# Kernel optimization log

Measured on AMD Instinct MI355X. Metric: run time of the kernel, lower is better.

## Reference

```python
import jax, jax.numpy as jnp
import numpy as np

N = 100000   # num_nodes
E = 1600000  # num_edges
DIN = 128
H1 = 256
H2 = 128
SLOPE = 0.01  # torch leaky_relu default negative slope


def _gcn_conv(h, W, b, src, dst):
    # GCNConv: add self-loops, symmetric deg^-1/2 normalization, linear transform, scatter-add, bias
    hw = h @ W  # [N, out]
    loops = jnp.arange(N)
    s = jnp.concatenate([src, loops])
    d = jnp.concatenate([dst, loops])
    deg = jax.ops.segment_sum(jnp.ones(s.shape[0], dtype=hw.dtype), d, num_segments=N)
    dis = jnp.where(deg > 0, jax.lax.rsqrt(deg), 0.0)
    msg = hw[s] * (dis[s] * dis[d])[:, None]
    return jax.ops.segment_sum(msg, d, num_segments=N) + b


def _gru_cell(x, h, Wih, Whh, bih, bhh):
    # torch.nn.GRUCell semantics; weight layout [3H, in], gate order r, z, n
    gi = x @ Wih.T + bih
    gh = h @ Whh.T + bhh
    ir, iz, inn = jnp.split(gi, 3, axis=-1)
    hr, hz, hn = jnp.split(gh, 3, axis=-1)
    r = jax.nn.sigmoid(ir + hr)
    z = jax.nn.sigmoid(iz + hz)
    n = jnp.tanh(inn + r * hn)
    return (1.0 - z) * n + z * h


def setup_inputs() -> dict:
    key = jax.random.key(0)
    ks = jax.random.split(key, 24)
    rn = lambda k, shape, s=0.05: (jax.random.normal(k, shape) * s).astype(jnp.float32)
    return {
        "x": rn(ks[0], (N, DIN), 1.0),
        "edge_index": jax.random.randint(ks[1], (2, E), 0, N, dtype=jnp.int32),
        "prev0": rn(ks[2], (N, H1), 1.0),
        "prev1": rn(ks[3], (N, H2), 1.0),
        "Wp1": rn(ks[4], (DIN, 256)), "bp1": jnp.zeros((256,), jnp.float32),
        "Wp2": rn(ks[5], (256, 128)), "bp2": jnp.zeros((128,), jnp.float32),
        "Wc1": rn(ks[6], (128, H1)), "bc1": jnp.zeros((H1,), jnp.float32),
        "Wc2": rn(ks[7], (H1, H2)), "bc2": jnp.zeros((H2,), jnp.float32),
        "Wih1": rn(ks[8], (3 * H1, H1)), "Whh1": rn(ks[9], (3 * H1, H1)),
        "bih1": jnp.zeros((3 * H1,), jnp.float32), "bhh1": jnp.zeros((3 * H1,), jnp.float32),
        "Wih2": rn(ks[10], (3 * H2, H2)), "Whh2": rn(ks[11], (3 * H2, H2)),
        "bih2": jnp.zeros((3 * H2,), jnp.float32), "bhh2": jnp.zeros((3 * H2,), jnp.float32),
        "Wpost": rn(ks[12], (H2, 2)), "bpost": jnp.zeros((2,), jnp.float32),
    }


def reference(x, edge_index, prev0, prev1, Wp1, bp1, Wp2, bp2, Wc1, bc1, Wc2, bc2,
              Wih1, Whh1, bih1, bhh1, Wih2, Whh2, bih2, bhh2, Wpost, bpost):
    src, dst = edge_index[0], edge_index[1]
    # preprocess MLP (dropout p=0 => identity)
    h = jax.nn.leaky_relu(x @ Wp1 + bp1, SLOPE)
    h = jax.nn.leaky_relu(h @ Wp2 + bp2, SLOPE)
    # GCN layer 1 + GRU temporal update
    h = jax.nn.leaky_relu(_gcn_conv(h, Wc1, bc1, src, dst), SLOPE)
    h = _gru_cell(h, prev0, Wih1, Whh1, bih1, bhh1)
    emb0 = h
    # GCN layer 2 + GRU temporal update
    h = jax.nn.leaky_relu(_gcn_conv(h, Wc2, bc2, src, dst), SLOPE)
    h = _gru_cell(h, prev1, Wih2, Whh2, bih2, bhh2)
    emb1 = h
    # postprocess and reduce
    out = jnp.sum(h @ Wpost + bpost, axis=-1)  # [N]
    return out, emb0, emb1
```

## Files before the change

### kernel.cpp

```cpp
#include <hip/hip_runtime.h>
#include <cstdint>
#include <cstddef>

typedef __bf16 bf16x8 __attribute__((ext_vector_type(8)));
typedef float f32x4 __attribute__((ext_vector_type(4)));
typedef unsigned short us16;

__device__ __forceinline__ float lrelu(float v) { return v >= 0.0f ? v : 0.01f * v; }
__device__ __forceinline__ float fsigmoid(float x) {
  x = fminf(fmaxf(x, -30.0f), 30.0f);
  return 1.0f / (1.0f + __expf(-x));
}
__device__ __forceinline__ float ftanh(float x) {
  x = fminf(fmaxf(x, -15.0f), 15.0f);
  float e = __expf(2.0f * x);
  return (e - 1.0f) / (e + 1.0f);
}
__device__ __forceinline__ us16 f2b(float f) {
  unsigned int u = __builtin_bit_cast(unsigned int, f);
  u = (u + 0x7fffu + ((u >> 16) & 1u)) >> 16;
  return (us16)u;
}
__device__ __forceinline__ float b2f(us16 h) {
  unsigned int u = ((unsigned int)h) << 16;
  return __builtin_bit_cast(float, u);
}
__device__ __forceinline__ unsigned pk2(float a, float b) {
  return (unsigned)f2b(a) | ((unsigned)f2b(b) << 16);
}
__device__ __forceinline__ void unp8(int4 v, float* t) {
  unsigned a = (unsigned)v.x, b = (unsigned)v.y, c = (unsigned)v.z, d = (unsigned)v.w;
  t[0] = b2f((us16)(a & 0xffff)); t[1] = b2f((us16)(a >> 16));
  t[2] = b2f((us16)(b & 0xffff)); t[3] = b2f((us16)(b >> 16));
  t[4] = b2f((us16)(c & 0xffff)); t[5] = b2f((us16)(c >> 16));
  t[6] = b2f((us16)(d & 0xffff)); t[7] = b2f((us16)(d >> 16));
}

__device__ __forceinline__ void stage16(const us16* gsrc, us16* ldst) {
  __builtin_amdgcn_global_load_lds(
      (const __attribute__((address_space(1))) unsigned int*)(const void*)gsrc,
      (__attribute__((address_space(3))) unsigned int*)(void*)ldst, 16, 0, 0);
}
__device__ __forceinline__ bf16x8 frag_rd(const us16* base, int row, int byte_in_row) {
  int byte = row * 128 + (byte_in_row ^ ((row & 7) << 4));
  return *(const bf16x8*)((const char*)base + byte);
}
__device__ __forceinline__ bf16x8 frd32(const us16* tilebase, int row, int ck16) {
  int slot = ck16 ^ ((row >> 1) & 3);
  return *(const bf16x8*)(tilebase + row * 32 + slot * 8);
}

__global__ void k_deg(const int* __restrict__ dst, int* __restrict__ indeg, int E) {
  int e = blockIdx.x * 256 + threadIdx.x;
  if (e < E) atomicAdd(&indeg[dst[e]], 1);
}

__global__ __launch_bounds__(1024) void k_scan1(const int* __restrict__ v, int* __restrict__ rp,
                                                int* __restrict__ part, float* __restrict__ dis, int n) {
  __shared__ int wsum[16];
  int base = blockIdx.x << 10;
  int t = threadIdx.x, lane = t & 63, wv = t >> 6;
  int val = (base + t < n) ? v[base + t] : 0;
  if (base + t < n) dis[base + t] = rsqrtf((float)(val + 1));
  int s = val;
  #pragma unroll
  for (int off = 1; off < 64; off <<= 1) {
    int u = __shfl_up(s, off);
    if (lane >= off) s += u;
  }
  if (lane == 63) wsum[wv] = s;
  __syncthreads();
  int wadd = 0;
  #pragma unroll
  for (int w = 0; w < 16; ++w) wadd += (w < wv) ? wsum[w] : 0;
  if (base + t < n) rp[base + t] = wadd + s - val;
  if (t == 0) {
    int tot = 0;
    #pragma unroll
    for (int w = 0; w < 16; ++w) tot += wsum[w];
    part[blockIdx.x] = tot;
  }
}

__global__ __launch_bounds__(1024) void k_scan2(int* __restrict__ p, int nc) {
  __shared__ int wsum[16];
  int t = threadIdx.x, lane = t & 63, wv = t >> 6;
  int val = (t < nc) ? p[t] : 0;
  int s = val;
  #pragma unroll
  for (int off = 1; off < 64; off <<= 1) {
    int u = __shfl_up(s, off);
    if (lane >= off) s += u;
  }
  if (lane == 63) wsum[wv] = s;
  __syncthreads();
  int wadd = 0;
  #pragma unroll
  for (int w = 0; w < 16; ++w) wadd += (w < wv) ? wsum[w] : 0;
  if (t < nc) p[t] = wadd + s - val;
}

__global__ void k_scan3(int* __restrict__ rp, const int* __restrict__ part,
                        int* __restrict__ cursor, int n, int total) {
  int i = blockIdx.x * 256 + threadIdx.x;
  if (i < n) {
    int v = rp[i] + part[i >> 10];
    rp[i] = v;
    cursor[i] = v;
  } else if (i == n) {
    rp[n] = total;
  }
}

__global__ void k_fill(const int* __restrict__ src, const int* __restrict__ dst,
                       const float* __restrict__ dis, int* __restrict__ cursor,
                       int* __restrict__ csrc, float* __restrict__ cw, int E) {
  int e = blockIdx.x * 256 + threadIdx.x;
  if (e >= E) return;
  int s = src[e], d = dst[e];
  int pos = atomicAdd(&cursor[d], 1);
  csrc[pos] = s;
  cw[pos] = dis[s] * dis[d];
}

__global__ void k_cast(const float* __restrict__ in, us16* __restrict__ out, int n) {
  int i = (blockIdx.x * 256 + threadIdx.x) * 4;
  if (i >= n) return;
  float4 v = *(const float4*)(in + i);
  *(ushort4*)(out + i) = make_ushort4(f2b(v.x), f2b(v.y), f2b(v.z), f2b(v.w));
}

__global__ void k_prepw(const float* __restrict__ Wih1, const float* __restrict__ Whh1,
                        const float* __restrict__ Wih2, const float* __restrict__ Whh2,
                        const float* __restrict__ Wp1, const float* __restrict__ Wp2,
                        const float* __restrict__ Wc1, const float* __restrict__ Wc2,
                        us16* __restrict__ Wih1b, us16* __restrict__ Whh1b,
                        us16* __restrict__ Wih2b, us16* __restrict__ Whh2b,
                        us16* __restrict__ WtP1, us16* __restrict__ WtP2,
                        us16* __restrict__ WtC1, us16* __restrict__ WtC2) {
  int e = blockIdx.x * 256 + threadIdx.x;
  if (e < 196608) { Wih1b[e] = f2b(Wih1[e]); return; }
  e -= 196608;
  if (e < 196608) { Whh1b[e] = f2b(Whh1[e]); return; }
  e -= 196608;
  if (e < 49152) { Wih2b[e] = f2b(Wih2[e]); return; }
  e -= 49152;
  if (e < 49152) { Whh2b[e] = f2b(Whh2[e]); return; }
  e -= 49152;
  if (e < 32768) { int r = e & 127, c = e >> 7; WtP1[e] = f2b(Wp1[(size_t)r * 256 + c]); return; }
  e -= 32768;
  if (e < 32768) { int r = e & 255, c = e >> 8; WtP2[e] = f2b(Wp2[(size_t)r * 128 + c]); return; }
  e -= 32768;
  if (e < 32768) { int r = e & 127, c = e >> 7; WtC1[e] = f2b(Wc1[(size_t)r * 256 + c]); return; }
  e -= 32768;
  if (e < 32768) { int r = e & 255, c = e >> 8; WtC2[e] = f2b(Wc2[(size_t)r * 128 + c]); }
}

template<int ACT, int BIAS>
__global__ __launch_bounds__(256) void k_mm(const us16* __restrict__ A,
                                            const us16* __restrict__ Bt,
                                            const float* __restrict__ bias,
                                            us16* __restrict__ Cb,
                                            int M, int K, int Nc, int ny) {
  __shared__ __align__(16) us16 lds[2][2 * 8192];
  const int bm = (blockIdx.x / ny) * 128;
  const int bn = (blockIdx.x % ny) * 128;
  const int tid = threadIdx.x;
  const int lane = tid & 63;
  const int wave = tid >> 6;
  const int wm = (wave >> 1) * 64;
  const int wn = (wave & 1) * 64;
  const int lr = lane & 15;
  const int lk = lane >> 4;
  const int srow = lane >> 3;
  const int schk = (lane & 7) ^ srow;
  f32x4 acc[4][4] = {};

  auto stage = [&](int k0, us16* buf) {
    #pragma unroll
    for (int it = 0; it < 4; ++it) {
      int r8 = (wave * 4 + it) * 8;
      int ar = bm + r8 + srow; if (ar >= M) ar = M - 1;
      stage16(A + (size_t)ar * K + k0 + schk * 8, buf + r8 * 64);
      stage16(Bt + (size_t)(bn + r8 + srow) * K + k0 + schk * 8, buf + 8192 + r8 * 64);
    }
  };

  const int nk = K >> 6;
  stage(0, lds[0]);
  for (int t = 0; t < nk; ++t) {
    us16* cur = lds[t & 1];
    __syncthreads();
    if (t + 1 < nk) stage((t + 1) << 6, lds[(t + 1) & 1]);
    #pragma unroll
    for (int kk = 0; kk < 2; ++kk) {
      bf16x8 af[4], bq[4];
      #pragma unroll
      for (int i = 0; i < 4; ++i) af[i] = frag_rd(cur, wm + i * 16 + lr, kk * 64 + lk * 16);
      #pragma unroll
      for (int j = 0; j < 4; ++j) bq[j] = frag_rd(cur + 8192, wn + j * 16 + lr, kk * 64 + lk * 16);
      #pragma unroll
      for (int i = 0; i < 4; ++i)
        #pragma unroll
        for (int j = 0; j < 4; ++j)
          acc[i][j] = __builtin_amdgcn_mfma_f32_16x16x32_bf16(af[i], bq[j], acc[i][j], 0, 0, 0);
    }
  }
  float bb[4];
  #pragma unroll
  for (int j = 0; j < 4; ++j) bb[j] = BIAS ? bias[bn + wn + j * 16 + lr] : 0.0f;
  #pragma unroll
  for (int i = 0; i < 4; ++i) {
    #pragma unroll
    for (int q = 0; q < 4; ++q) {
      int row = bm + wm + i * 16 + lk * 4 + q;
      if (row < M) {
        #pragma unroll
        for (int j = 0; j < 4; ++j) {
          int col = bn + wn + j * 16 + lr;
          float v = acc[i][j][q] + bb[j];
          if (ACT) v = lrelu(v);
          Cb[(size_t)row * Nc + col] = f2b(v);
        }
      }
    }
  }
}

template<int ACT>
__global__ __launch_bounds__(256) void k_agg128(const us16* __restrict__ hw, const int* __restrict__ rp,
                                                const int* __restrict__ csrc, const float* __restrict__ cw,
                                                const float* __restrict__ dis, const float* __restrict__ bias,
                                                us16* __restrict__ outp, int M) {
  int node = blockIdx.x * 16 + (threadIdx.x >> 4);
  int l = threadIdx.x & 15;
  if (node >= M) return;
  const us16* base = hw + l * 8;
  float acc[8], t0[8], t1[8], t2[8], t3[8];
  float dn = dis[node];
  float sw = dn * dn;
  {
    int4 v = *(const int4*)(base + (size_t)node * 128);
    unp8(v, t0);
    #pragma unroll
    for (int j = 0; j < 8; ++j) acc[j] = t0[j] * sw;
  }
  int e = rp[node], e1 = rp[node + 1];
  for (; e + 4 <= e1; e += 4) {
    int s0 = csrc[e], s1 = csrc[e + 1], s2 = csrc[e + 2], s3 = csrc[e + 3];
    float w0 = cw[e], w1 = cw[e + 1], w2 = cw[e + 2], w3 = cw[e + 3];
    int4 v0 = *(const int4*)(base + (size_t)s0 * 128);
    int4 v1 = *(const int4*)(base + (size_t)s1 * 128);
    int4 v2 = *(const int4*)(base + (size_t)s2 * 128);
    int4 v3 = *(const int4*)(base + (size_t)s3 * 128);
    unp8(v0, t0); unp8(v1, t1); unp8(v2, t2); unp8(v3, t3);
    #pragma unroll
    for (int j = 0; j < 8; ++j) acc[j] = fmaf(w0, t0[j], acc[j]);
    #pragma unroll
    for (int j = 0; j < 8; ++j) acc[j] = fmaf(w1, t1[j], acc[j]);
    #pragma unroll
    for (int j = 0; j < 8; ++j) acc[j] = fmaf(w2, t2[j], acc[j]);
    #pragma unroll
    for (int j = 0; j < 8; ++j) acc[j] = fmaf(w3, t3[j], acc[j]);
  }
  for (; e < e1; ++e) {
    int s0 = csrc[e];
    float w0 = cw[e];
    int4 v0 = *(const int4*)(base + (size_t)s0 * 128);
    unp8(v0, t0);
    #pragma unroll
    for (int j = 0; j < 8; ++j) acc[j] = fmaf(w0, t0[j], acc[j]);
  }
  if (ACT) {
    float4 b0 = *(const float4*)(bias + l * 8);
    float4 b1 = *(const float4*)(bias + l * 8 + 4);
    float bb[8] = {b0.x, b0.y, b0.z, b0.w, b1.x, b1.y, b1.z, b1.w};
    #pragma unroll
    for (int j = 0; j < 8; ++j) acc[j] = lrelu(acc[j] + bb[j]);
  }
  int4 o;
  o.x = (int)pk2(acc[0], acc[1]);
  o.y = (int)pk2(acc[2], acc[3]);
  o.z = (int)pk2(acc[4], acc[5]);
  o.w = (int)pk2(acc[6], acc[7]);
  *(int4*)(outp + (size_t)node * 128 + l * 8) = o;
}

template<int H, int WB, int PH>
__global__ __launch_bounds__(512) void k_fgru(const us16* __restrict__ xb, const us16* __restrict__ hb,
                                              const us16* __restrict__ Wih, const us16* __restrict__ Whh,
                                              const float* __restrict__ bih, const float* __restrict__ bhh,
                                              float* __restrict__ emb, us16* __restrict__ embb,
                                              const float* __restrict__ Wpost, const float* __restrict__ bpost,
                                              float* __restrict__ outv, int M, int ny) {
  __shared__ __align__(16) us16 lds[2][14336];
  const int nwg = gridDim.x;
  int bid = blockIdx.x;
  {
    int q8 = nwg >> 3, r8 = nwg & 7;
    int xc = bid & 7, ix = bid >> 3;
    bid = (xc < r8 ? xc * (q8 + 1) : r8 * (q8 + 1) + (xc - r8) * q8) + ix;
  }
  const int bn = (bid % ny) * 32;
  const int bm = (bid / ny) * 128;
  const int tid = threadIdx.x;
  const int lane = tid & 63, wave = tid >> 6;
  const int pair = wave >> 1;
  const int role = wave & 1;
  const int wm = pair * 32;
  const int lr = lane & 15, lk = lane >> 4;
  const int sl_row = lane >> 2;
  const int sl_chk = (lane & 3) ^ ((lane >> 3) & 3);

  f32x4 acc[3][2][2] = {};

  auto stage_step = [&](int k0, us16* buf) {
    #pragma unroll
    for (int it = 0; it < 4; ++it) {
      int m = wave * 4 + it;
      if (m >= 28) break;
      const us16* src;
      us16* dst;
      if (m < 16) {
        int r0 = (m & 7) * 16;
        int ar = bm + r0 + sl_row; if (ar >= M) ar = M - 1;
        src = (m < 8 ? xb : hb) + (size_t)ar * H + k0 + sl_chk * 8;
        dst = buf + (m < 8 ? 0 : 4096) + r0 * 32;
      } else {
        int wi = m - 16;
        int g6 = wi >> 1;
        int r0 = (wi & 1) * 16;
        const us16* W = (g6 < 3) ? Wih : Whh;
        int gg = (g6 < 3) ? g6 : g6 - 3;
        src = W + (size_t)(gg * H + bn + r0 + sl_row) * H + k0 + sl_chk * 8;
        dst = buf + 8192 + g6 * 1024 + r0 * 32;
      }
      stage16(src, dst);
    }
  };

  const int nk = H >> 5;
  stage_step(0, lds[0]);
  for (int t = 0; t < nk; ++t) {
    us16* cur = lds[t & 1];
    __syncthreads();
    if (t + 1 < nk) stage_step((t + 1) << 5, lds[(t + 1) & 1]);
    const us16* at = cur + (role ? 4096 : 0);
    bf16x8 a0 = frd32(at, wm + lr, lk);
    bf16x8 a1 = frd32(at, wm + 16 + lr, lk);
    #pragma unroll
    for (int g = 0; g < 3; ++g) {
      const us16* wt = cur + 8192 + (role * 3 + g) * 1024;
      bf16x8 b0 = frd32(wt, lr, lk);
      bf16x8 b1 = frd32(wt, 16 + lr, lk);
      acc[g][0][0] = __builtin_amdgcn_mfma_f32_16x16x32_bf16(a0, b0, acc[g][0][0], 0, 0, 0);
      acc[g][0][1] = __builtin_amdgcn_mfma_f32_16x16x32_bf16(a0, b1, acc[g][0][1], 0, 0, 0);
      acc[g][1][0] = __builtin_amdgcn_mfma_f32_16x16x32_bf16(a1, b0, acc[g][1][0], 0, 0, 0);
      acc[g][1][1] = __builtin_amdgcn_mfma_f32_16x16x32_bf16(a1, b1, acc[g][1][1], 0, 0, 0);
    }
  }
  __syncthreads();
  float* xch = (float*)&lds[0][0];
  if (role) {
    #pragma unroll
    for (int g = 0; g < 3; ++g)
      #pragma unroll
      for (int i = 0; i < 2; ++i)
        #pragma unroll
        for (int j = 0; j < 2; ++j)
          *(f32x4*)&xch[((((pair * 3 + g) * 2 + i) * 2 + j) * 64 + lane) * 4] = acc[g][i][j];
  }
  __syncthreads();
  if (!role) {
    float part[2][4] = {};
    #pragma unroll
    for (int j = 0; j < 2; ++j) {
      int col = bn + j * 16 + lr;
      float bir = bih[col], biz = bih[H + col], bin = bih[2 * H + col];
      float bhr = bhh[col], bhz = bhh[H + col], bhn = bhh[2 * H + col];
      float wps = 0.0f;
      if (PH) wps = Wpost[2 * col] + Wpost[2 * col + 1];
      #pragma unroll
      for (int i = 0; i < 2; ++i) {
        f32x4 gr_ = *(const f32x4*)&xch[((((pair * 3 + 0) * 2 + i) * 2 + j) * 64 + lane) * 4];
        f32x4 gz_ = *(const f32x4*)&xch[((((pair * 3 + 1) * 2 + i) * 2 + j) * 64 + lane) * 4];
        f32x4 gn_ = *(const f32x4*)&xch[((((pair * 3 + 2) * 2 + i) * 2 + j) * 64 + lane) * 4];
        #pragma unroll
        for (int q = 0; q < 4; ++q) {
          int row = bm + wm + i * 16 + lk * 4 + q;
          if (row < M) {
            float r = fsigmoid(acc[0][i][j][q] + bir + gr_[q] + bhr);
            float z = fsigmoid(acc[1][i][j][q] + biz + gz_[q] + bhz);
            float n = ftanh(acc[2][i][j][q] + bin + r * (gn_[q] + bhn));
            float hv = b2f(hb[(size_t)row * H + col]);
            float o = (1.0f - z) * n + z * hv;
            emb[(size_t)row * H + col] = o;
            if (WB) embb[(size_t)row * H + col] = f2b(o);
            if (PH) part[i][q] += o * wps;
          }
        }
      }
    }
    if (PH) {
      float bsum = bpost[0] + bpost[1];
      #pragma unroll
      for (int i = 0; i < 2; ++i)
        #pragma unroll
        for (int q = 0; q < 4; ++q) {
          float v = part[i][q];
          v += __shfl_xor(v, 1); v += __shfl_xor(v, 2);
          v += __shfl_xor(v, 4); v += __shfl_xor(v, 8);
          int row = bm + wm + i * 16 + lk * 4 + q;
          if (lr == 0 && row < M)
            atomicAdd(&outv[row], v + (bn == 0 ? bsum : 0.0f));
        }
    }
  }
}

extern "C" void kernel_launch(void* const* d_in, const int* in_sizes, int n_in,
                              void* d_out, int out_size, void* d_ws, size_t ws_size,
                              hipStream_t stream) {
  const float* x     = (const float*)d_in[0];
  const int*   ei    = (const int*)d_in[1];
  const float* prev0 = (const float*)d_in[2];
  const float* prev1 = (const float*)d_in[3];
  const float* Wp1   = (const float*)d_in[4];
  const float* bp1   = (const float*)d_in[5];
  const float* Wp2   = (const float*)d_in[6];
  const float* bp2   = (const float*)d_in[7];
  const float* Wc1   = (const float*)d_in[8];
  const float* bc1   = (const float*)d_in[9];
  const float* Wc2   = (const float*)d_in[10];
  const float* bc2   = (const float*)d_in[11];
  const float* Wih1  = (const float*)d_in[12];
  const float* Whh1  = (const float*)d_in[13];
  const float* bih1  = (const float*)d_in[14];
  const float* bhh1  = (const float*)d_in[15];
  const float* Wih2  = (const float*)d_in[16];
  const float* Whh2  = (const float*)d_in[17];
  const float* bih2  = (const float*)d_in[18];
  const float* bhh2  = (const float*)d_in[19];
  const float* Wpost = (const float*)d_in[20];
  const float* bpost = (const float*)d_in[21];

  const int N = in_sizes[0] / 128;
  const int E = in_sizes[1] / 2;
  const int* srcp = ei;
  const int* dstp = ei + E;

  char* wsb = (char*)d_ws;
  size_t off = 0;
  auto alloc = [&](size_t bytes) -> void* {
    void* p = wsb + off;
    off = (off + bytes + 255) & ~(size_t)255;
    return p;
  };
  float* dis    = (float*)alloc((size_t)N * 4);
  int*   indeg  = (int*)alloc((size_t)N * 4);
  int*   rp     = (int*)alloc((size_t)(N + 1) * 4);
  int*   part   = (int*)alloc((size_t)1024 * 4);
  int*   cursor = (int*)alloc((size_t)N * 4);
  int*   csrc   = (int*)alloc((size_t)E * 4);
  float* cw     = (float*)alloc((size_t)E * 4);
  us16* xb    = (us16*)alloc((size_t)N * 128 * 2);
  us16* p0b   = (us16*)alloc((size_t)N * 256 * 2);
  us16* p1b   = (us16*)alloc((size_t)N * 128 * 2);
  us16* WtP1  = (us16*)alloc((size_t)256 * 128 * 2);
  us16* WtP2  = (us16*)alloc((size_t)128 * 256 * 2);
  us16* WtC1  = (us16*)alloc((size_t)256 * 128 * 2);
  us16* WtC2  = (us16*)alloc((size_t)128 * 256 * 2);
  us16* Wih1b = (us16*)alloc((size_t)768 * 256 * 2);
  us16* Whh1b = (us16*)alloc((size_t)768 * 256 * 2);
  us16* Wih2b = (us16*)alloc((size_t)384 * 128 * 2);
  us16* Whh2b = (us16*)alloc((size_t)384 * 128 * 2);
  us16* bufA  = (us16*)alloc((size_t)N * 256 * 2);
  us16* bufB  = (us16*)alloc((size_t)N * 128 * 2);
  us16* bufD  = (us16*)alloc((size_t)N * 128 * 2);
  us16* emb0b = (us16*)alloc((size_t)N * 256 * 2);
  (void)ws_size; (void)n_in; (void)out_size;

  float* outv = (float*)d_out;
  float* emb0 = outv + N;
  float* emb1 = emb0 + (size_t)N * 256;

  auto cg = [](long n) { return (unsigned)((n / 4 + 255) / 256); };

  hipMemsetAsync(outv, 0, (size_t)N * 4, stream);

  k_cast<<<cg((long)N * 128), 256, 0, stream>>>(x, xb, N * 128);
  k_cast<<<cg((long)N * 256), 256, 0, stream>>>(prev0, p0b, N * 256);
  k_cast<<<cg((long)N * 128), 256, 0, stream>>>(prev1, p1b, N * 128);
  k_prepw<<<2432, 256, 0, stream>>>(Wih1, Whh1, Wih2, Whh2, Wp1, Wp2, Wc1, Wc2,
                                    Wih1b, Whh1b, Wih2b, Whh2b, WtP1, WtP2, WtC1, WtC2);

  hipMemsetAsync(indeg, 0, (size_t)N * 4, stream);
  k_deg<<<(E + 255) / 256, 256, 0, stream>>>(dstp, indeg, E);
  const int NC = (N + 1023) / 1024;
  k_scan1<<<NC, 1024, 0, stream>>>(indeg, rp, part, dis, N);
  k_scan2<<<1, 1024, 0, stream>>>(part, NC);
  k_scan3<<<(N + 256) / 256, 256, 0, stream>>>(rp, part, cursor, N, E);
  k_fill<<<(E + 255) / 256, 256, 0, stream>>>(srcp, dstp, dis, cursor, csrc, cw, E);

  const int MB = (N + 127) / 128;
  const int AB = (N + 15) / 16;

  k_mm<1, 1><<<MB * 2, 256, 0, stream>>>(xb, WtP1, bp1, bufA, N, 128, 256, 2);
  k_mm<1, 1><<<MB, 256, 0, stream>>>(bufA, WtP2, bp2, bufB, N, 256, 128, 1);
  k_agg128<0><<<AB, 256, 0, stream>>>(bufB, rp, csrc, cw, dis, nullptr, bufD, N);
  k_mm<1, 1><<<MB * 2, 256, 0, stream>>>(bufD, WtC1, bc1, bufA, N, 128, 256, 2);
  k_fgru<256, 1, 0><<<MB * 8, 512, 0, stream>>>(bufA, p0b, Wih1b, Whh1b, bih1, bhh1,
                                                emb0, emb0b, nullptr, nullptr, nullptr, N, 8);
  k_mm<0, 0><<<MB, 256, 0, stream>>>(emb0b, WtC2, nullptr, bufB, N, 256, 128, 1);
  k_agg128<1><<<AB, 256, 0, stream>>>(bufB, rp, csrc, cw, dis, bc2, bufD, N);
  k_fgru<128, 0, 1><<<MB * 4, 512, 0, stream>>>(bufD, p1b, Wih2b, Whh2b, bih2, bhh2,
                                                emb1, nullptr, Wpost, bpost, outv, N, 4);
}
```

Before: 803.1 us.

## Preload full weight tiles into LDS and stream activations directly from global

Both the dense GEMM kernel and the fused GRU kernel stop double-buffering A and B tiles through LDS with async global-to-LDS loads per K step. Instead, each block loads its entire weight slice into swizzled LDS once, then reads activation fragments straight from global memory into registers across a fully unrolled K loop. This removes the per-step barriers and the LDS round trip for activations. In exchange, LDS use per block grows (up to 96 KB for H=256 GRU), which may cut occupancy, and uncoalesced direct A loads may add global-memory latency with no overlap.

```diff
diff --git a/kernel.cpp b/kernel.cpp
--- a/kernel.cpp
+++ b/kernel.cpp
@@ -34,20 +34,6 @@
   t[2] = b2f((us16)(b & 0xffff)); t[3] = b2f((us16)(b >> 16));
   t[4] = b2f((us16)(c & 0xffff)); t[5] = b2f((us16)(c >> 16));
   t[6] = b2f((us16)(d & 0xffff)); t[7] = b2f((us16)(d >> 16));
-}
-
-__device__ __forceinline__ void stage16(const us16* gsrc, us16* ldst) {
-  __builtin_amdgcn_global_load_lds(
-      (const __attribute__((address_space(1))) unsigned int*)(const void*)gsrc,
-      (__attribute__((address_space(3))) unsigned int*)(void*)ldst, 16, 0, 0);
-}
-__device__ __forceinline__ bf16x8 frag_rd(const us16* base, int row, int byte_in_row) {
-  int byte = row * 128 + (byte_in_row ^ ((row & 7) << 4));
-  return *(const bf16x8*)((const char*)base + byte);
-}
-__device__ __forceinline__ bf16x8 frd32(const us16* tilebase, int row, int ck16) {
-  int slot = ck16 ^ ((row >> 1) & 3);
-  return *(const bf16x8*)(tilebase + row * 32 + slot * 8);
 }
 
 __global__ void k_deg(const int* __restrict__ dst, int* __restrict__ indeg, int E) {
@@ -156,13 +142,13 @@
   if (e < 32768) { int r = e & 255, c = e >> 8; WtC2[e] = f2b(Wc2[(size_t)r * 128 + c]); }
 }
 
-template<int ACT, int BIAS>
+template<int ACT, int BIAS, int K>
 __global__ __launch_bounds__(256) void k_mm(const us16* __restrict__ A,
                                             const us16* __restrict__ Bt,
                                             const float* __restrict__ bias,
                                             us16* __restrict__ Cb,
-                                            int M, int K, int Nc, int ny) {
-  __shared__ __align__(16) us16 lds[2][2 * 8192];
+                                            int M, int Nc, int ny) {
+  __shared__ __align__(16) us16 wl[128 * K];
   const int bm = (blockIdx.x / ny) * 128;
   const int bn = (blockIdx.x % ny) * 128;
   const int tid = threadIdx.x;
@@ -172,39 +158,42 @@
   const int wn = (wave & 1) * 64;
   const int lr = lane & 15;
   const int lk = lane >> 4;
-  const int srow = lane >> 3;
-  const int schk = (lane & 7) ^ srow;
+
+  constexpr int CHB = K / 8;
+  #pragma unroll
+  for (int it = 0; it < (128 * CHB) / 256; ++it) {
+    int idx = it * 256 + tid;
+    int cir = idx & (CHB - 1);
+    int col = idx / CHB;
+    int4 v = *(const int4*)(Bt + (size_t)(bn + col) * K + cir * 8);
+    size_t db = (((size_t)col * K + cir * 8) * 2) ^ (size_t)((col & 7) << 4);
+    *(int4*)((char*)wl + db) = v;
+  }
+  __syncthreads();
+
+  const us16* ap[4];
+  #pragma unroll
+  for (int i = 0; i < 4; ++i) {
+    int r = bm + wm + i * 16 + lr; if (r >= M) r = M - 1;
+    ap[i] = A + (size_t)r * K + lk * 8;
+  }
   f32x4 acc[4][4] = {};
-
-  auto stage = [&](int k0, us16* buf) {
-    #pragma unroll
-    for (int it = 0; it < 4; ++it) {
-      int r8 = (wave * 4 + it) * 8;
-      int ar = bm + r8 + srow; if (ar >= M) ar = M - 1;
-      stage16(A + (size_t)ar * K + k0 + schk * 8, buf + r8 * 64);
-      stage16(Bt + (size_t)(bn + r8 + srow) * K + k0 + schk * 8, buf + 8192 + r8 * 64);
+  #pragma unroll
+  for (int kk = 0; kk < K / 32; ++kk) {
+    bf16x8 af[4], bq[4];
+    #pragma unroll
+    for (int i = 0; i < 4; ++i) af[i] = *(const bf16x8*)(ap[i] + kk * 32);
+    #pragma unroll
+    for (int j = 0; j < 4; ++j) {
+      int col = wn + j * 16 + lr;
+      size_t db = (((size_t)col * K + kk * 32 + lk * 8) * 2) ^ (size_t)((col & 7) << 4);
+      bq[j] = *(const bf16x8*)((const char*)wl + db);
     }
-  };
-
-  const int nk = K >> 6;
-  stage(0, lds[0]);
-  for (int t = 0; t < nk; ++t) {
-    us16* cur = lds[t & 1];
-    __syncthreads();
-    if (t + 1 < nk) stage((t + 1) << 6, lds[(t + 1) & 1]);
-    #pragma unroll
-    for (int kk = 0; kk < 2; ++kk) {
-      bf16x8 af[4], bq[4];
+    #pragma unroll
+    for (int i = 0; i < 4; ++i)
       #pragma unroll
-      for (int i = 0; i < 4; ++i) af[i] = frag_rd(cur, wm + i * 16 + lr, kk * 64 + lk * 16);
-      #pragma unroll
-      for (int j = 0; j < 4; ++j) bq[j] = frag_rd(cur + 8192, wn + j * 16 + lr, kk * 64 + lk * 16);
-      #pragma unroll
-      for (int i = 0; i < 4; ++i)
-        #pragma unroll
-        for (int j = 0; j < 4; ++j)
-          acc[i][j] = __builtin_amdgcn_mfma_f32_16x16x32_bf16(af[i], bq[j], acc[i][j], 0, 0, 0);
-    }
+      for (int j = 0; j < 4; ++j)
+        acc[i][j] = __builtin_amdgcn_mfma_f32_16x16x32_bf16(af[i], bq[j], acc[i][j], 0, 0, 0);
   }
   float bb[4];
   #pragma unroll
@@ -293,7 +282,7 @@
                                               float* __restrict__ emb, us16* __restrict__ embb,
                                               const float* __restrict__ Wpost, const float* __restrict__ bpost,
                                               float* __restrict__ outv, int M, int ny) {
-  __shared__ __align__(16) us16 lds[2][14336];
+  __shared__ __align__(16) us16 wl[192 * H];
   const int nwg = gridDim.x;
   int bid = blockIdx.x;
   {
@@ -307,60 +296,51 @@
   const int lane = tid & 63, wave = tid >> 6;
   const int pair = wave >> 1;
   const int role = wave & 1;
-  const int wm = pair * 32;
   const int lr = lane & 15, lk = lane >> 4;
-  const int sl_row = lane >> 2;
-  const int sl_chk = (lane & 3) ^ ((lane >> 3) & 3);
+
+  constexpr int CHR = H / 8;
+  #pragma unroll
+  for (int it = 0; it < (192 * CHR) / 512; ++it) {
+    int idx = it * 512 + tid;
+    int cir = idx & (CHR - 1);
+    int row = idx / CHR;
+    int g6 = row >> 5, c = row & 31;
+    const us16* W = (g6 < 3) ? Wih : Whh;
+    int gg = (g6 < 3) ? g6 : g6 - 3;
+    int4 v = *(const int4*)(W + (size_t)(gg * H + bn + c) * H + cir * 8);
+    size_t db = (((size_t)row * H + cir * 8) * 2) ^ (size_t)((c & 7) << 4);
+    *(int4*)((char*)wl + db) = v;
+  }
+  __syncthreads();
+
+  const us16* abase = role ? hb : xb;
+  int ra0 = bm + pair * 32 + lr;      if (ra0 >= M) ra0 = M - 1;
+  int ra1 = bm + pair * 32 + 16 + lr; if (ra1 >= M) ra1 = M - 1;
+  const us16* ap0 = abase + (size_t)ra0 * H + lk * 8;
+  const us16* ap1 = abase + (size_t)ra1 * H + lk * 8;
 
   f32x4 acc[3][2][2] = {};
-
-  auto stage_step = [&](int k0, us16* buf) {
-    #pragma unroll
-    for (int it = 0; it < 4; ++it) {
-      int m = wave * 4 + it;
-      if (m >= 28) break;
-      const us16* src;
-      us16* dst;
-      if (m < 16) {
-        int r0 = (m & 7) * 16;
-        int ar = bm + r0 + sl_row; if (ar >= M) ar = M - 1;
-        src = (m < 8 ? xb : hb) + (size_t)ar * H + k0 + sl_chk * 8;
-        dst = buf + (m < 8 ? 0 : 4096) + r0 * 32;
-      } else {
-        int wi = m - 16;
-        int g6 = wi >> 1;
-        int r0 = (wi & 1) * 16;
-        const us16* W = (g6 < 3) ? Wih : Whh;
-        int gg = (g6 < 3) ? g6 : g6 - 3;
-        src = W + (size_t)(gg * H + bn + r0 + sl_row) * H + k0 + sl_chk * 8;
-        dst = buf + 8192 + g6 * 1024 + r0 * 32;
-      }
-      stage16(src, dst);
-    }
-  };
-
-  const int nk = H >> 5;
-  stage_step(0, lds[0]);
-  for (int t = 0; t < nk; ++t) {
-    us16* cur = lds[t & 1];
-    __syncthreads();
-    if (t + 1 < nk) stage_step((t + 1) << 5, lds[(t + 1) & 1]);
-    const us16* at = cur + (role ? 4096 : 0);
-    bf16x8 a0 = frd32(at, wm + lr, lk);
-    bf16x8 a1 = frd32(at, wm + 16 + lr, lk);
+  #pragma unroll
+  for (int t = 0; t < H / 32; ++t) {
+    bf16x8 a0 = *(const bf16x8*)(ap0 + t * 32);
+    bf16x8 a1 = *(const bf16x8*)(ap1 + t * 32);
     #pragma unroll
     for (int g = 0; g < 3; ++g) {
-      const us16* wt = cur + 8192 + (role * 3 + g) * 1024;
-      bf16x8 b0 = frd32(wt, lr, lk);
-      bf16x8 b1 = frd32(wt, 16 + lr, lk);
+      int g6 = role * 3 + g;
+      int c0 = lr, c1 = 16 + lr;
+      size_t db0 = (((size_t)(g6 * 32 + c0) * H + t * 32 + lk * 8) * 2) ^ (size_t)((c0 & 7) << 4);
+      size_t db1 = (((size_t)(g6 * 32 + c1) * H + t * 32 + lk * 8) * 2) ^ (size_t)((c1 & 7) << 4);
+      bf16x8 b0 = *(const bf16x8*)((const char*)wl + db0);
+      bf16x8 b1 = *(const bf16x8*)((const char*)wl + db1);
       acc[g][0][0] = __builtin_amdgcn_mfma_f32_16x16x32_bf16(a0, b0, acc[g][0][0], 0, 0, 0);
       acc[g][0][1] = __builtin_amdgcn_mfma_f32_16x16x32_bf16(a0, b1, acc[g][0][1], 0, 0, 0);
       acc[g][1][0] = __builtin_amdgcn_mfma_f32_16x16x32_bf16(a1, b0, acc[g][1][0], 0, 0, 0);
       acc[g][1][1] = __builtin_amdgcn_mfma_f32_16x16x32_bf16(a1, b1, acc[g][1][1], 0, 0, 0);
     }
   }
-  __syncthreads();
-  float* xch = (float*)&lds[0][0];
+
+  __syncthreads();
+  float* xch = (float*)&wl[0];
   if (role) {
     #pragma unroll
     for (int g = 0; g < 3; ++g)
@@ -387,7 +367,7 @@
         f32x4 gn_ = *(const f32x4*)&xch[((((pair * 3 + 2) * 2 + i) * 2 + j) * 64 + lane) * 4];
         #pragma unroll
         for (int q = 0; q < 4; ++q) {
-          int row = bm + wm + i * 16 + lk * 4 + q;
+          int row = bm + pair * 32 + i * 16 + lk * 4 + q;
           if (row < M) {
             float r = fsigmoid(acc[0][i][j][q] + bir + gr_[q] + bhr);
             float z = fsigmoid(acc[1][i][j][q] + biz + gz_[q] + bhz);
@@ -410,7 +390,7 @@
           float v = part[i][q];
           v += __shfl_xor(v, 1); v += __shfl_xor(v, 2);
           v += __shfl_xor(v, 4); v += __shfl_xor(v, 8);
-          int row = bm + wm + i * 16 + lk * 4 + q;
+          int row = bm + pair * 32 + i * 16 + lk * 4 + q;
           if (lr == 0 && row < M)
             atomicAdd(&outv[row], v + (bn == 0 ? bsum : 0.0f));
         }
@@ -505,13 +485,13 @@
   const int MB = (N + 127) / 128;
   const int AB = (N + 15) / 16;
 
-  k_mm<1, 1><<<MB * 2, 256, 0, stream>>>(xb, WtP1, bp1, bufA, N, 128, 256, 2);
-  k_mm<1, 1><<<MB, 256, 0, stream>>>(bufA, WtP2, bp2, bufB, N, 256, 128, 1);
+  k_mm<1, 1, 128><<<MB * 2, 256, 0, stream>>>(xb, WtP1, bp1, bufA, N, 256, 2);
+  k_mm<1, 1, 256><<<MB, 256, 0, stream>>>(bufA, WtP2, bp2, bufB, N, 128, 1);
   k_agg128<0><<<AB, 256, 0, stream>>>(bufB, rp, csrc, cw, dis, nullptr, bufD, N);
-  k_mm<1, 1><<<MB * 2, 256, 0, stream>>>(bufD, WtC1, bc1, bufA, N, 128, 256, 2);
+  k_mm<1, 1, 128><<<MB * 2, 256, 0, stream>>>(bufD, WtC1, bc1, bufA, N, 256, 2);
   k_fgru<256, 1, 0><<<MB * 8, 512, 0, stream>>>(bufA, p0b, Wih1b, Whh1b, bih1, bhh1,
                                                 emb0, emb0b, nullptr, nullptr, nullptr, N, 8);
-  k_mm<0, 0><<<MB, 256, 0, stream>>>(emb0b, WtC2, nullptr, bufB, N, 256, 128, 1);
+  k_mm<0, 0, 256><<<MB, 256, 0, stream>>>(emb0b, WtC2, nullptr, bufB, N, 128, 1);
   k_agg128<1><<<AB, 256, 0, stream>>>(bufB, rp, csrc, cw, dis, bc2, bufD, N);
   k_fgru<128, 0, 1><<<MB * 4, 512, 0, stream>>>(bufD, p1b, Wih2b, Whh2b, bih2, bhh2,
                                                 emb1, nullptr, Wpost, bpost, outv, N, 4);
```

Measured after the change: 839.4 us. 1.05x slower.

## Load GRU MFMA operands directly from global memory instead of LDS staging

Applied to the files above, without the earlier changes.

The fused GRU kernel drops its double-buffered LDS staging (global_load_lds plus __syncthreads each k-step) and instead has each wave read its A rows and weight rows straight from global memory into MFMA fragments, with a fully unrolled k loop. LDS is now used only for the gate exchange between wave pairs. This removes per-step barriers and LDS traffic, but weight tiles are no longer shared across waves through LDS. Each wave reads them independently, and the reads are 16-byte strided row loads that depend on L1/L2 hits rather than coalesced staging.

```diff
diff --git a/kernel.cpp b/kernel.cpp
--- a/kernel.cpp
+++ b/kernel.cpp
@@ -44,10 +44,6 @@
 __device__ __forceinline__ bf16x8 frag_rd(const us16* base, int row, int byte_in_row) {
   int byte = row * 128 + (byte_in_row ^ ((row & 7) << 4));
   return *(const bf16x8*)((const char*)base + byte);
-}
-__device__ __forceinline__ bf16x8 frd32(const us16* tilebase, int row, int ck16) {
-  int slot = ck16 ^ ((row >> 1) & 3);
-  return *(const bf16x8*)(tilebase + row * 32 + slot * 8);
 }
 
 __global__ void k_deg(const int* __restrict__ dst, int* __restrict__ indeg, int E) {
@@ -293,7 +289,7 @@
                                               float* __restrict__ emb, us16* __restrict__ embb,
                                               const float* __restrict__ Wpost, const float* __restrict__ bpost,
                                               float* __restrict__ outv, int M, int ny) {
-  __shared__ __align__(16) us16 lds[2][14336];
+  __shared__ __align__(16) float xch[12288];
   const int nwg = gridDim.x;
   int bid = blockIdx.x;
   {
@@ -307,60 +303,39 @@
   const int lane = tid & 63, wave = tid >> 6;
   const int pair = wave >> 1;
   const int role = wave & 1;
-  const int wm = pair * 32;
   const int lr = lane & 15, lk = lane >> 4;
-  const int sl_row = lane >> 2;
-  const int sl_chk = (lane & 3) ^ ((lane >> 3) & 3);
+
+  const us16* abase = role ? hb : xb;
+  int ra0 = bm + pair * 32 + lr;      if (ra0 >= M) ra0 = M - 1;
+  int ra1 = bm + pair * 32 + 16 + lr; if (ra1 >= M) ra1 = M - 1;
+  const us16* ap0 = abase + (size_t)ra0 * H + lk * 8;
+  const us16* ap1 = abase + (size_t)ra1 * H + lk * 8;
+  const us16* wbase = role ? Whh : Wih;
+  const us16* bp0[3];
+  const us16* bp1[3];
+  #pragma unroll
+  for (int g = 0; g < 3; ++g) {
+    bp0[g] = wbase + (size_t)(g * H + bn + lr) * H + lk * 8;
+    bp1[g] = wbase + (size_t)(g * H + bn + 16 + lr) * H + lk * 8;
+  }
 
   f32x4 acc[3][2][2] = {};
-
-  auto stage_step = [&](int k0, us16* buf) {
-    #pragma unroll
-    for (int it = 0; it < 4; ++it) {
-      int m = wave * 4 + it;
-      if (m >= 28) break;
-      const us16* src;
-      us16* dst;
-      if (m < 16) {
-        int r0 = (m & 7) * 16;
-        int ar = bm + r0 + sl_row; if (ar >= M) ar = M - 1;
-        src = (m < 8 ? xb : hb) + (size_t)ar * H + k0 + sl_chk * 8;
-        dst = buf + (m < 8 ? 0 : 4096) + r0 * 32;
-      } else {
-        int wi = m - 16;
-        int g6 = wi >> 1;
-        int r0 = (wi & 1) * 16;
-        const us16* W = (g6 < 3) ? Wih : Whh;
-        int gg = (g6 < 3) ? g6 : g6 - 3;
-        src = W + (size_t)(gg * H + bn + r0 + sl_row) * H + k0 + sl_chk * 8;
-        dst = buf + 8192 + g6 * 1024 + r0 * 32;
-      }
-      stage16(src, dst);
-    }
-  };
-
-  const int nk = H >> 5;
-  stage_step(0, lds[0]);
-  for (int t = 0; t < nk; ++t) {
-    us16* cur = lds[t & 1];
-    __syncthreads();
-    if (t + 1 < nk) stage_step((t + 1) << 5, lds[(t + 1) & 1]);
-    const us16* at = cur + (role ? 4096 : 0);
-    bf16x8 a0 = frd32(at, wm + lr, lk);
-    bf16x8 a1 = frd32(at, wm + 16 + lr, lk);
+  #pragma unroll
+  for (int t = 0; t < H / 32; ++t) {
+    bf16x8 a0 = *(const bf16x8*)(ap0 + t * 32);
+    bf16x8 a1 = *(const bf16x8*)(ap1 + t * 32);
     #pragma unroll
     for (int g = 0; g < 3; ++g) {
-      const us16* wt = cur + 8192 + (role * 3 + g) * 1024;
-      bf16x8 b0 = frd32(wt, lr, lk);
-      bf16x8 b1 = frd32(wt, 16 + lr, lk);
+      bf16x8 b0 = *(const bf16x8*)(bp0[g] + t * 32);
+      bf16x8 b1 = *(const bf16x8*)(bp1[g] + t * 32);
       acc[g][0][0] = __builtin_amdgcn_mfma_f32_16x16x32_bf16(a0, b0, acc[g][0][0], 0, 0, 0);
       acc[g][0][1] = __builtin_amdgcn_mfma_f32_16x16x32_bf16(a0, b1, acc[g][0][1], 0, 0, 0);
       acc[g][1][0] = __builtin_amdgcn_mfma_f32_16x16x32_bf16(a1, b0, acc[g][1][0], 0, 0, 0);
       acc[g][1][1] = __builtin_amdgcn_mfma_f32_16x16x32_bf16(a1, b1, acc[g][1][1], 0, 0, 0);
     }
   }
+
   __syncthreads();
-  float* xch = (float*)&lds[0][0];
   if (role) {
     #pragma unroll
     for (int g = 0; g < 3; ++g)
@@ -387,7 +362,7 @@
         f32x4 gn_ = *(const f32x4*)&xch[((((pair * 3 + 2) * 2 + i) * 2 + j) * 64 + lane) * 4];
         #pragma unroll
         for (int q = 0; q < 4; ++q) {
-          int row = bm + wm + i * 16 + lk * 4 + q;
+          int row = bm + pair * 32 + i * 16 + lk * 4 + q;
           if (row < M) {
             float r = fsigmoid(acc[0][i][j][q] + bir + gr_[q] + bhr);
             float z = fsigmoid(acc[1][i][j][q] + biz + gz_[q] + bhz);
@@ -410,7 +385,7 @@
           float v = part[i][q];
           v += __shfl_xor(v, 1); v += __shfl_xor(v, 2);
           v += __shfl_xor(v, 4); v += __shfl_xor(v, 8);
-          int row = bm + wm + i * 16 + lk * 4 + q;
+          int row = bm + pair * 32 + i * 16 + lk * 4 + q;
           if (lr == 0 && row < M)
             atomicAdd(&outv[row], v + (bn == 0 ? bsum : 0.0f));
         }
```

Result: slower. 1.026 ms (+27.8%).
